# Optimization experiments

Measured on AMD Instinct MI355X. Metric: run time of the kernel, lower is better.

Reference implementation:

```python
import jax, jax.numpy as jnp
import numpy as np

H, T, D = 16, 2048, 1024
DH = D // H  # 64


def setup_inputs() -> dict:
    key = jax.random.key(0)
    ks = jax.random.split(key, 6)
    state = jax.random.normal(ks[0], (H, DH, DH), jnp.float32) * 0.02  # per-head recurrent state
    x = jax.random.normal(ks[1], (T, D), jnp.float32)
    done = jax.random.uniform(ks[2], (T,)) < (4.0 / T)  # sparse episode-reset flags (bool)
    w_qkv = jax.random.normal(ks[3], (D, 3 * D), jnp.float32) / np.sqrt(D)
    b_qkv = jnp.zeros((3 * D,), jnp.float32)
    w_out = jax.random.normal(ks[4], (D, D), jnp.float32) / np.sqrt(D)
    b_out = jnp.zeros((D,), jnp.float32)
    return {"state": state, "x": x, "done": done, "w_qkv": w_qkv,
            "b_qkv": b_qkv, "w_out": w_out, "b_out": b_out}


def _mha_forward(state, x, done, w_qkv, b_qkv, w_out, b_out):
    # qkv projection; einops 'T (QKV H Dh) -> QKV H T Dh'
    qkv = (x @ w_qkv + b_qkv).reshape(T, 3, H, DH).transpose(1, 2, 0, 3)
    q, k, v = qkv[0], qkv[1], qkv[2]  # each (H, T, Dh)

    cum = jnp.cumsum(done.astype(jnp.int32))  # inclusive cumsum, as in done.cumsum()
    before_first = cum == 0            # tokens before first reset (attend to carried state)
    after_last = cum == cum[-1]        # tokens after last reset (feed new state)
    done_any = cum[-1] > 0

    # make_attn_mask(done): causal AND no reset index i with s < i <= t.
    # The scanned mask equals: causal & (cum[t] == cum[s]) (same-segment).
    t_idx = jnp.arange(T)
    mask = (t_idx[:, None] >= t_idx[None, :]) & (cum[:, None] == cum[None, :])  # (T, T)

    attn = jnp.where(mask[None], jnp.einsum('htd,hsd->hts', q, k), 0.0)  # mask * (q @ k.T)
    q_bef = q * before_first[None, :, None]
    out = jnp.einsum('hts,hsd->htd', attn, v) + jnp.einsum('htd,hde->hte', q_bef, state)

    k_aft = k * after_last[None, :, None]
    v_aft = v * after_last[None, :, None]
    s_new = jnp.einsum('htd,hte->hde', k_aft, v_aft)  # k_aft.T @ v_aft per head
    new_state = jnp.where(done_any, s_new, state + s_new)

    # 'H T Dh -> T (H Dh)' then output projection
    x_out = out.transpose(1, 0, 2).reshape(T, D) @ w_out + b_out
    return new_state, x_out


def reference(state, x, done, w_qkv, b_qkv, w_out, b_out):
    return _mha_forward(state, x, done, w_qkv, b_qkv, w_out, b_out)
```

## Files before the change

### kernel.cpp

```cpp
#include <hip/hip_runtime.h>

#define TT 2048
#define DD 1024
#define HH 16
#define DH 64
#define QKV_N 3072
#define QKW 2048

typedef __attribute__((ext_vector_type(8))) short bf16x8;
typedef __attribute__((ext_vector_type(4))) short short4v;
typedef __attribute__((ext_vector_type(4))) float f32x4;

__device__ inline short f2bf(float f) {
    union { float f; unsigned u; } v; v.f = f;
    unsigned r = v.u + 0x7fff + ((v.u >> 16) & 1);
    return (short)(r >> 16);
}

__device__ inline f32x4 mfma16(bf16x8 a, bf16x8 b, f32x4 c) {
    return __builtin_amdgcn_mfma_f32_16x16x32_bf16(a, b, c, 0, 0, 0);
}

__device__ __forceinline__ void gload16(const void* g, void* l) {
    __builtin_amdgcn_global_load_lds(
        (const __attribute__((address_space(1))) unsigned int*)g,
        (__attribute__((address_space(3))) unsigned int*)l, 16, 0, 0);
}

__device__ void transpose_tile(const float* __restrict__ in, short* __restrict__ out,
                               int R, int C, int r0, int c0, float (*tile)[65]) {
    int tid = threadIdx.x;
#pragma unroll
    for (int p = 0; p < 4; ++p) {
        int ch = tid + p * 256;
        int r = ch >> 4, c4 = (ch & 15) * 4;
        float4 v = *(const float4*)&in[(size_t)(r0 + r) * C + c0 + c4];
        tile[r][c4] = v.x; tile[r][c4 + 1] = v.y; tile[r][c4 + 2] = v.z; tile[r][c4 + 3] = v.w;
    }
    __syncthreads();
#pragma unroll
    for (int p = 0; p < 2; ++p) {
        int ch = tid + p * 256;
        int c = ch >> 3, r8 = (ch & 7) * 8;
        short tmp[8];
#pragma unroll
        for (int i = 0; i < 8; ++i) tmp[i] = f2bf(tile[r8 + i][c]);
        *(float4*)&out[(size_t)(c0 + c) * R + r0 + r8] = *(float4*)tmp;
    }
}

__global__ __launch_bounds__(256) void prep_kernel(const float* __restrict__ x,
                                                   const float* __restrict__ w_qkv,
                                                   const float* __restrict__ w_out,
                                                   const float* __restrict__ state,
                                                   const int* __restrict__ done,
                                                   short* __restrict__ x_bf,
                                                   short* __restrict__ wqT,
                                                   short* __restrict__ woT,
                                                   short* __restrict__ stT,
                                                   float* __restrict__ stout,
                                                   int* __restrict__ seg,
                                                   int* __restrict__ totalp,
                                                   int* __restrict__ aux) {
    __shared__ float tile[64][65];
    __shared__ int scanbuf[2048 + 512 + 1];
    int b = blockIdx.x;
    int tid = threadIdx.x;
    if (b < 1024) {
        int i = (b * 256 + tid) * 8;
        float4 a = *(const float4*)&x[i];
        float4 c = *(const float4*)&x[i + 4];
        short tmp[8] = {f2bf(a.x), f2bf(a.y), f2bf(a.z), f2bf(a.w),
                        f2bf(c.x), f2bf(c.y), f2bf(c.z), f2bf(c.w)};
        *(float4*)&x_bf[i] = *(float4*)tmp;
    } else if (b < 1792) {
        int bb = b - 1024;
        transpose_tile(w_qkv, wqT, DD, QKV_N, (bb & 15) * 64, (bb >> 4) * 64, tile);
    } else if (b < 2048) {
        int bb = b - 1792;
        transpose_tile(w_out, woT, DD, DD, (bb & 15) * 64, (bb >> 4) * 64, tile);
    } else if (b < 2064) {
        int h = b - 2048;
        transpose_tile(state + (size_t)h * 4096, stT + (size_t)h * 4096, DH, DH, 0, 0, tile);
    } else if (b < 2128) {
        __shared__ int anyf;
        if (tid == 0) anyf = 0;
        __syncthreads();
        int acc = 0;
#pragma unroll
        for (int i = 0; i < 8; ++i) acc |= done[tid * 8 + i];
        if (acc) anyf = 1;
        __syncthreads();
        int f = ((b - 2064) * 256 + tid) * 4;
        float4 v = anyf ? make_float4(0.f, 0.f, 0.f, 0.f) : *(const float4*)&state[f];
        *(float4*)&stout[f] = v;
    } else {
        int* segl = scanbuf;
        int* part = scanbuf + 2048;
        int* excl = scanbuf + 2304;
        int base = tid * 8;
        int local[8];
        int run = 0;
#pragma unroll
        for (int i = 0; i < 8; ++i) { run += (done[base + i] != 0) ? 1 : 0; local[i] = run; }
        part[tid] = run;
        __syncthreads();
        if (tid < 64) {
            int p4[4];
#pragma unroll
            for (int i = 0; i < 4; ++i) p4[i] = part[tid * 4 + i];
            int s = p4[0] + p4[1] + p4[2] + p4[3];
            int v = s;
#pragma unroll
            for (int off = 1; off < 64; off <<= 1) {
                int u = __shfl_up(v, off);
                if (tid >= off) v += u;
            }
            int ex = v - s;
#pragma unroll
            for (int i = 0; i < 4; ++i) { excl[tid * 4 + i] = ex; ex += p4[i]; }
            if (tid == 63) { totalp[0] = v; scanbuf[2560] = v; }
        }
        __syncthreads();
        int off = excl[tid];
#pragma unroll
        for (int i = 0; i < 8; ++i) {
            int sv = off + local[i];
            seg[base + i] = sv;
            segl[base + i] = sv;
        }
        __syncthreads();
        if (tid < 33) {
            int target = (tid < 32) ? segl[tid * 64] : scanbuf[2560];
            int lo = 0, hi = 2047;
            while (lo < hi) { int mid = (lo + hi) >> 1; if (segl[mid] >= target) hi = mid; else lo = mid + 1; }
            aux[tid] = lo >> 6;
        }
    }
}

__global__ __launch_bounds__(256) void gemm_qkv(const short* __restrict__ A,
                                                const short* __restrict__ BT,
                                                const float* __restrict__ bias,
                                                short* __restrict__ qk,
                                                short* __restrict__ vt) {
    __shared__ __align__(16) short As[128 * 32];
    __shared__ __align__(16) short Bs[128 * 32];
    const int K = DD;
    int tid = threadIdx.x;
    int wave = tid >> 6, lane = tid & 63;
    int quad = lane >> 4, l15 = lane & 15;
    int m0 = blockIdx.x * 128, n0 = blockIdx.y * 128;
    int wr = (wave >> 1) * 64, wc = (wave & 1) * 64;

    int srow = wave * 16 + (lane >> 2);
    int scol = (lane & 3) * 8;
    const short* Ag = A + (size_t)(m0 + srow) * K + scol;
    const short* Bg = BT + (size_t)(n0 + srow) * K + scol;
    short* As0 = &As[(wave * 16) * 32];
    short* As1 = &As[(64 + wave * 16) * 32];
    short* Bs0 = &Bs[(wave * 16) * 32];
    short* Bs1 = &Bs[(64 + wave * 16) * 32];

    f32x4 acc[4][4] = {};
    for (int k0 = 0; k0 < K; k0 += 32) {
        __syncthreads();
        gload16(Ag + k0, As0);
        gload16(Ag + (size_t)64 * K + k0, As1);
        gload16(Bg + k0, Bs0);
        gload16(Bg + (size_t)64 * K + k0, Bs1);
        __syncthreads();
        bf16x8 af[4], bfr[4];
#pragma unroll
        for (int i = 0; i < 4; ++i) {
            af[i]  = *(const bf16x8*)&As[(wr + i * 16 + l15) * 32 + quad * 8];
            bfr[i] = *(const bf16x8*)&Bs[(wc + i * 16 + l15) * 32 + quad * 8];
        }
#pragma unroll
        for (int i = 0; i < 4; ++i)
#pragma unroll
            for (int j = 0; j < 4; ++j)
                acc[i][j] = mfma16(af[i], bfr[j], acc[i][j]);
    }

    if (n0 < 2048) {
#pragma unroll
        for (int i = 0; i < 4; ++i)
#pragma unroll
            for (int j = 0; j < 4; ++j)
#pragma unroll
                for (int r = 0; r < 4; ++r) {
                    int row = m0 + wr + i * 16 + quad * 4 + r;
                    int col = n0 + wc + j * 16 + l15;
                    qk[(size_t)row * QKW + col] = f2bf(acc[i][j][r] + bias[col]);
                }
    } else {
#pragma unroll
        for (int j = 0; j < 4; ++j) {
            int col = n0 + wc + j * 16 + l15;
            float bv = bias[col];
            int eg = col - 2048;
            int hh = eg >> 6, e = eg & 63;
#pragma unroll
            for (int i = 0; i < 4; ++i) {
                int tb = m0 + wr + i * 16 + quad * 4;
                short4v pk;
#pragma unroll
                for (int r = 0; r < 4; ++r) pk[r] = f2bf(acc[i][j][r] + bv);
                *(short4v*)&vt[(size_t)hh * (DH * TT) + (size_t)e * TT + tb] = pk;
            }
        }
    }
}

__global__ __launch_bounds__(256) void attn_mfma(const short* __restrict__ qk,
                                                 const short* __restrict__ vt,
                                                 const short* __restrict__ stT,
                                                 const int* __restrict__ seg,
                                                 const int* __restrict__ totalp,
                                                 const int* __restrict__ aux,
                                                 short* __restrict__ outb,
                                                 float* __restrict__ part,
                                                 float* __restrict__ nsout) {
    __shared__ __align__(16) short Kh[2][64 * 32];
    __shared__ __align__(16) short Vh[2][64 * 32];
    __shared__ __align__(16) short Qh[2][128 * 32];
    __shared__ __align__(16) short Ss[128 * 72];

    int h = blockIdx.x, tb = blockIdx.y, sc = blockIdx.z;
    int t0 = tb * 128;
    int tid = threadIdx.x, wave = tid >> 6, lane = tid & 63;
    int quad = lane >> 4, l15 = lane & 15;
    int myt = wave * 32;
    const short* vbase = vt + (size_t)h * (DH * TT);

    if (sc == 4) {
        int total = totalp[0];
        int myd = wave * 16;
#pragma unroll
        for (int cc = 0; cc < 2; ++cc) {
            int ct = tb * 2 + cc;
            if (ct < aux[32]) continue;
            int t0c = ct * 64;
            bool keep = (seg[t0c + lane] == total);
            const short* src = qk + (size_t)(t0c + lane) * QKW + 1024 + h * DH + myd;
            union { float4 f; short s[8]; } u0, u1;
            u0.f = keep ? *(const float4*)src : make_float4(0.f, 0.f, 0.f, 0.f);
            u1.f = keep ? *(const float4*)(src + 8) : make_float4(0.f, 0.f, 0.f, 0.f);
            short* dst = (lane < 32) ? &Kh[0][lane] : &Kh[1][lane - 32];
#pragma unroll
            for (int i = 0; i < 8; ++i) {
                dst[(myd + i) * 32] = u0.s[i];
                dst[(myd + 8 + i) * 32] = u1.s[i];
            }
            bf16x8 a0 = *(const bf16x8*)&Kh[0][(myd + l15) * 32 + quad * 8];
            bf16x8 a1 = *(const bf16x8*)&Kh[1][(myd + l15) * 32 + quad * 8];
            f32x4 acc2[4] = {};
#pragma unroll
            for (int j = 0; j < 4; ++j) {
                const short* vrow = vbase + (size_t)(j * 16 + l15) * TT + t0c + quad * 8;
                bf16x8 b0 = *(const bf16x8*)vrow;
                bf16x8 b1 = *(const bf16x8*)(vrow + 32);
                acc2[j] = mfma16(a0, b0, acc2[j]);
                acc2[j] = mfma16(a1, b1, acc2[j]);
            }
            float* oh = nsout + (size_t)h * 4096;
#pragma unroll
            for (int j = 0; j < 4; ++j)
#pragma unroll
                for (int r = 0; r < 4; ++r)
                    atomicAdd(&oh[(myd + quad * 4 + r) * DH + j * 16 + l15], acc2[j][r]);
        }
        return;
    }

    int st0 = aux[2 * tb];
    int sc_lo = st0 >> 3, sc_hi = (2 * tb + 1) >> 3;
    if (sc < sc_lo || sc > sc_hi) return;
    bool direct = (sc_lo == sc_hi);
    int st_lo = (st0 > sc * 8) ? st0 : sc * 8;
    int st_hi = (2 * tb + 1 < sc * 8 + 7) ? 2 * tb + 1 : sc * 8 + 7;

    {
        int srow = (lane >> 2);
        int chunk = (lane & 3);
#pragma unroll
        for (int h2 = 0; h2 < 2; ++h2)
#pragma unroll
            for (int q = 0; q < 2; ++q) {
                int row = myt + q * 16 + srow;
                gload16(qk + (size_t)(t0 + row) * QKW + h * DH + h2 * 32 + chunk * 8,
                        &Qh[h2][(myt + q * 16) * 32]);
            }
    }
    __syncthreads();

    bf16x8 af[2][2];
#pragma unroll
    for (int i = 0; i < 2; ++i)
#pragma unroll
        for (int h2 = 0; h2 < 2; ++h2)
            af[i][h2] = *(const bf16x8*)&Qh[h2][(myt + i * 16 + l15) * 32 + quad * 8];

    int tg[2][4], segt[2][4];
#pragma unroll
    for (int i = 0; i < 2; ++i)
#pragma unroll
        for (int r = 0; r < 4; ++r) {
            tg[i][r] = t0 + myt + i * 16 + quad * 4 + r;
            segt[i][r] = seg[tg[i][r]];
        }

    f32x4 acc[2][4] = {};
    if (sc == sc_lo && seg[t0] == 0) {
        const short* sb = stT + (size_t)h * 4096;
#pragma unroll
        for (int j = 0; j < 4; ++j)
#pragma unroll
            for (int h2 = 0; h2 < 2; ++h2) {
                bf16x8 b = *(const bf16x8*)(sb + (j * 16 + l15) * 64 + h2 * 32 + quad * 8);
#pragma unroll
                for (int i = 0; i < 2; ++i)
                    acc[i][j] = mfma16(af[i][h2], b, acc[i][j]);
            }
#pragma unroll
        for (int i = 0; i < 2; ++i)
#pragma unroll
            for (int r = 0; r < 4; ++r)
                if (segt[i][r] != 0)
#pragma unroll
                    for (int j = 0; j < 4; ++j) acc[i][j][r] = 0.f;
    }

    int srow = wave * 16 + (lane >> 2);
    int chunk = (lane & 3);
    const short* kg = qk + 1024 + h * DH;

    for (int st = st_lo; st <= st_hi; ++st) {
        int s0 = st * 64;
        __syncthreads();
        gload16(kg + (size_t)(s0 + srow) * QKW + chunk * 8,        &Kh[0][(wave * 16) * 32]);
        gload16(kg + (size_t)(s0 + srow) * QKW + 32 + chunk * 8,   &Kh[1][(wave * 16) * 32]);
        gload16(vbase + (size_t)srow * TT + s0 + chunk * 8,        &Vh[0][(wave * 16) * 32]);
        gload16(vbase + (size_t)srow * TT + s0 + 32 + chunk * 8,   &Vh[1][(wave * 16) * 32]);
        __syncthreads();

        int segs[4], sg[4];
#pragma unroll
        for (int j = 0; j < 4; ++j) { sg[j] = s0 + j * 16 + l15; segs[j] = seg[sg[j]]; }

        f32x4 sacc[2][4] = {};
#pragma unroll
        for (int j = 0; j < 4; ++j)
#pragma unroll
            for (int h2 = 0; h2 < 2; ++h2) {
                bf16x8 kb = *(const bf16x8*)&Kh[h2][(j * 16 + l15) * 32 + quad * 8];
#pragma unroll
                for (int i = 0; i < 2; ++i)
                    sacc[i][j] = mfma16(af[i][h2], kb, sacc[i][j]);
            }
#pragma unroll
        for (int i = 0; i < 2; ++i)
#pragma unroll
            for (int j = 0; j < 4; ++j)
#pragma unroll
                for (int r = 0; r < 4; ++r) {
                    bool ok = (segs[j] == segt[i][r]) && (sg[j] <= tg[i][r]);
                    Ss[(myt + i * 16 + quad * 4 + r) * 72 + j * 16 + l15] =
                        ok ? f2bf(sacc[i][j][r]) : (short)0;
                }
        bf16x8 sf[2][2];
#pragma unroll
        for (int i = 0; i < 2; ++i)
#pragma unroll
            for (int h2 = 0; h2 < 2; ++h2)
                sf[i][h2] = *(const bf16x8*)&Ss[(myt + i * 16 + l15) * 72 + h2 * 32 + quad * 8];
#pragma unroll
        for (int j = 0; j < 4; ++j)
#pragma unroll
            for (int h2 = 0; h2 < 2; ++h2) {
                bf16x8 vb = *(const bf16x8*)&Vh[h2][(j * 16 + l15) * 32 + quad * 8];
#pragma unroll
                for (int i = 0; i < 2; ++i)
                    acc[i][j] = mfma16(sf[i][h2], vb, acc[i][j]);
            }
    }

    if (direct) {
#pragma unroll
        for (int i = 0; i < 2; ++i)
#pragma unroll
            for (int j = 0; j < 4; ++j)
#pragma unroll
                for (int r = 0; r < 4; ++r)
                    outb[(size_t)tg[i][r] * DD + h * DH + j * 16 + l15] = f2bf(acc[i][j][r]);
    } else {
        float* pb = part + ((size_t)((h * 16 + tb) * 4 + sc)) * 8192;
#pragma unroll
        for (int i = 0; i < 2; ++i)
#pragma unroll
            for (int j = 0; j < 4; ++j)
#pragma unroll
                for (int r = 0; r < 4; ++r)
                    pb[(myt + i * 16 + quad * 4 + r) * 64 + j * 16 + l15] = acc[i][j][r];
    }
}

__global__ __launch_bounds__(256) void attn_reduce(const float* __restrict__ part,
                                                   const int* __restrict__ aux,
                                                   short* __restrict__ outb) {
    int h = blockIdx.x, tb = blockIdx.y;
    int sc_lo = aux[2 * tb] >> 3, sc_hi = (2 * tb + 1) >> 3;
    if (sc_lo == sc_hi) return;
    int t0 = tb * 128;
    int tid = threadIdx.x;
    const float* pb = part + ((size_t)(h * 16 + tb) * 4) * 8192;
#pragma unroll
    for (int p = 0; p < 8; ++p) {
        int idx = p * 256 + tid;
        int row = idx >> 4, c4 = (idx & 15) * 4;
        float4 acc = make_float4(0.f, 0.f, 0.f, 0.f);
        for (int sc = sc_lo; sc <= sc_hi; ++sc) {
            float4 v = *(const float4*)&pb[(size_t)sc * 8192 + row * 64 + c4];
            acc.x += v.x; acc.y += v.y; acc.z += v.z; acc.w += v.w;
        }
        short4v pk;
        pk[0] = f2bf(acc.x); pk[1] = f2bf(acc.y); pk[2] = f2bf(acc.z); pk[3] = f2bf(acc.w);
        *(short4v*)&outb[(size_t)(t0 + row) * DD + h * DH + c4] = pk;
    }
}

__global__ __launch_bounds__(256) void gemm_out(const short* __restrict__ A,
                                                const short* __restrict__ BT,
                                                const float* __restrict__ bias,
                                                float* __restrict__ Cout,
                                                int M, int N, int K) {
    __shared__ __align__(16) short As[128 * 32];
    __shared__ __align__(16) short Bs[128 * 32];
    int tid = threadIdx.x;
    int wave = tid >> 6, lane = tid & 63;
    int quad = lane >> 4, l15 = lane & 15;
    int m0 = blockIdx.x * 128, n0 = blockIdx.y * 128;
    int wr = (wave >> 1) * 64, wc = (wave & 1) * 64;

    int srow = wave * 16 + (lane >> 2);
    int scol = (lane & 3) * 8;
    const short* Ag = A + (size_t)(m0 + srow) * K + scol;
    const short* Bg = BT + (size_t)(n0 + srow) * K + scol;
    short* As0 = &As[(wave * 16) * 32];
    short* As1 = &As[(64 + wave * 16) * 32];
    short* Bs0 = &Bs[(wave * 16) * 32];
    short* Bs1 = &Bs[(64 + wave * 16) * 32];

    f32x4 acc[4][4] = {};
    for (int k0 = 0; k0 < K; k0 += 32) {
        __syncthreads();
        gload16(Ag + k0, As0);
        gload16(Ag + (size_t)64 * K + k0, As1);
        gload16(Bg + k0, Bs0);
        gload16(Bg + (size_t)64 * K + k0, Bs1);
        __syncthreads();
        bf16x8 af[4], bfr[4];
#pragma unroll
        for (int i = 0; i < 4; ++i) {
            af[i]  = *(const bf16x8*)&As[(wr + i * 16 + l15) * 32 + quad * 8];
            bfr[i] = *(const bf16x8*)&Bs[(wc + i * 16 + l15) * 32 + quad * 8];
        }
#pragma unroll
        for (int i = 0; i < 4; ++i)
#pragma unroll
            for (int j = 0; j < 4; ++j)
                acc[i][j] = mfma16(af[i], bfr[j], acc[i][j]);
    }
#pragma unroll
    for (int i = 0; i < 4; ++i)
#pragma unroll
        for (int j = 0; j < 4; ++j)
#pragma unroll
            for (int r = 0; r < 4; ++r) {
                int row = m0 + wr + i * 16 + quad * 4 + r;
                int col = n0 + wc + j * 16 + l15;
                Cout[(size_t)row * N + col] = acc[i][j][r] + bias[col];
            }
}

extern "C" void kernel_launch(void* const* d_in, const int* in_sizes, int n_in,
                              void* d_out, int out_size, void* d_ws, size_t ws_size,
                              hipStream_t stream) {
    const float* state = (const float*)d_in[0];
    const float* x     = (const float*)d_in[1];
    const int*   done  = (const int*)d_in[2];
    const float* w_qkv = (const float*)d_in[3];
    const float* b_qkv = (const float*)d_in[4];
    const float* w_out = (const float*)d_in[5];
    const float* b_out = (const float*)d_in[6];

    char* ws = (char*)d_ws;
    int*   seg    = (int*)ws;
    int*   totalp = (int*)(ws + 8192);
    int*   aux    = (int*)(ws + 8256);
    short* wqT    = (short*)(ws + 8448);
    short* woT    = (short*)(ws + 6299904);
    short* stT    = (short*)(ws + 8397056);
    short* qk     = (short*)(ws + 8528128);
    short* vt     = (short*)(ws + 16916736);
    short* xbf_outb = (short*)(ws + 21111040);
    float* part   = (float*)(ws + 25305344);

    float* new_state_out = (float*)d_out;
    float* x_out         = (float*)d_out + HH * DH * DH;

    prep_kernel<<<2129, 256, 0, stream>>>(x, w_qkv, w_out, state, done,
                                          xbf_outb, wqT, woT, stT,
                                          new_state_out, seg, totalp, aux);

    gemm_qkv<<<dim3(TT / 128, QKV_N / 128), 256, 0, stream>>>(
        xbf_outb, wqT, b_qkv, qk, vt);

    attn_mfma<<<dim3(HH, TT / 128, 5), 256, 0, stream>>>(
        qk, vt, stT, seg, totalp, aux, xbf_outb, part, new_state_out);

    attn_reduce<<<dim3(HH, TT / 128), 256, 0, stream>>>(part, aux, xbf_outb);

    gemm_out<<<dim3(TT / 128, DD / 128), 256, 0, stream>>>(
        xbf_outb, woT, b_out, x_out, TT, DD, DD);
}
```

Baseline: 161.9 us.

## Drop split-K attention partials and double-buffer K/V tiles in one pass

Removes the key-chunk split (grid z=5 with fp32 partials plus a separate reduce kernel). Each block now walks its whole key range in one pass and writes bf16 output directly. K/V tiles are double-buffered in shared memory so the next tile's loads overlap the current MFMA work. MFMA operands are swapped so the results come out transposed, which allows vectorized short4 stores and int4 segment loads. This saves one kernel launch and the partial-sum traffic, but long key ranges are no longer spread across blocks, which lowers parallelism for late query tiles.

Measured after the change: 163.5 us. Within noise of the previous version (+1.0%).

```diff
diff --git a/kernel.cpp b/kernel.cpp
--- a/kernel.cpp
+++ b/kernel.cpp
@@ -220,23 +220,24 @@
                                                  const int* __restrict__ totalp,
                                                  const int* __restrict__ aux,
                                                  short* __restrict__ outb,
-                                                 float* __restrict__ part,
                                                  float* __restrict__ nsout) {
-    __shared__ __align__(16) short Kh[2][64 * 32];
-    __shared__ __align__(16) short Vh[2][64 * 32];
     __shared__ __align__(16) short Qh[2][128 * 32];
+    __shared__ __align__(16) short Kh[2][2][64 * 32];
+    __shared__ __align__(16) short Vh[2][2][64 * 32];
     __shared__ __align__(16) short Ss[128 * 72];
 
-    int h = blockIdx.x, tb = blockIdx.y, sc = blockIdx.z;
+    int h = blockIdx.x, tb = blockIdx.y;
     int t0 = tb * 128;
     int tid = threadIdx.x, wave = tid >> 6, lane = tid & 63;
     int quad = lane >> 4, l15 = lane & 15;
     int myt = wave * 32;
     const short* vbase = vt + (size_t)h * (DH * TT);
 
-    if (sc == 4) {
+    if (blockIdx.z == 1) {
         int total = totalp[0];
         int myd = wave * 16;
+        short* KhS0 = Kh[0][0];
+        short* KhS1 = Kh[0][1];
 #pragma unroll
         for (int cc = 0; cc < 2; ++cc) {
             int ct = tb * 2 + cc;
@@ -247,14 +248,14 @@
             union { float4 f; short s[8]; } u0, u1;
             u0.f = keep ? *(const float4*)src : make_float4(0.f, 0.f, 0.f, 0.f);
             u1.f = keep ? *(const float4*)(src + 8) : make_float4(0.f, 0.f, 0.f, 0.f);
-            short* dst = (lane < 32) ? &Kh[0][lane] : &Kh[1][lane - 32];
+            short* dst = (lane < 32) ? &KhS0[lane] : &KhS1[lane - 32];
 #pragma unroll
             for (int i = 0; i < 8; ++i) {
                 dst[(myd + i) * 32] = u0.s[i];
                 dst[(myd + 8 + i) * 32] = u1.s[i];
             }
-            bf16x8 a0 = *(const bf16x8*)&Kh[0][(myd + l15) * 32 + quad * 8];
-            bf16x8 a1 = *(const bf16x8*)&Kh[1][(myd + l15) * 32 + quad * 8];
+            bf16x8 a0 = *(const bf16x8*)&KhS0[(myd + l15) * 32 + quad * 8];
+            bf16x8 a1 = *(const bf16x8*)&KhS1[(myd + l15) * 32 + quad * 8];
             f32x4 acc2[4] = {};
 #pragma unroll
             for (int j = 0; j < 4; ++j) {
@@ -275,100 +276,103 @@
     }
 
     int st0 = aux[2 * tb];
-    int sc_lo = st0 >> 3, sc_hi = (2 * tb + 1) >> 3;
-    if (sc < sc_lo || sc > sc_hi) return;
-    bool direct = (sc_lo == sc_hi);
-    int st_lo = (st0 > sc * 8) ? st0 : sc * 8;
-    int st_hi = (2 * tb + 1 < sc * 8 + 7) ? 2 * tb + 1 : sc * 8 + 7;
-
-    {
-        int srow = (lane >> 2);
-        int chunk = (lane & 3);
-#pragma unroll
-        for (int h2 = 0; h2 < 2; ++h2)
-#pragma unroll
-            for (int q = 0; q < 2; ++q) {
-                int row = myt + q * 16 + srow;
-                gload16(qk + (size_t)(t0 + row) * QKW + h * DH + h2 * 32 + chunk * 8,
-                        &Qh[h2][(myt + q * 16) * 32]);
-            }
-    }
-    __syncthreads();
-
-    bf16x8 af[2][2];
-#pragma unroll
-    for (int i = 0; i < 2; ++i)
-#pragma unroll
-        for (int h2 = 0; h2 < 2; ++h2)
-            af[i][h2] = *(const bf16x8*)&Qh[h2][(myt + i * 16 + l15) * 32 + quad * 8];
-
-    int tg[2][4], segt[2][4];
-#pragma unroll
-    for (int i = 0; i < 2; ++i)
-#pragma unroll
-        for (int r = 0; r < 4; ++r) {
-            tg[i][r] = t0 + myt + i * 16 + quad * 4 + r;
-            segt[i][r] = seg[tg[i][r]];
-        }
-
-    f32x4 acc[2][4] = {};
-    if (sc == sc_lo && seg[t0] == 0) {
-        const short* sb = stT + (size_t)h * 4096;
-#pragma unroll
-        for (int j = 0; j < 4; ++j)
-#pragma unroll
-            for (int h2 = 0; h2 < 2; ++h2) {
-                bf16x8 b = *(const bf16x8*)(sb + (j * 16 + l15) * 64 + h2 * 32 + quad * 8);
-#pragma unroll
-                for (int i = 0; i < 2; ++i)
-                    acc[i][j] = mfma16(af[i][h2], b, acc[i][j]);
-            }
-#pragma unroll
-        for (int i = 0; i < 2; ++i)
-#pragma unroll
-            for (int r = 0; r < 4; ++r)
-                if (segt[i][r] != 0)
-#pragma unroll
-                    for (int j = 0; j < 4; ++j) acc[i][j][r] = 0.f;
-    }
+    int st_hi = 2 * tb + 1;
 
     int srow = wave * 16 + (lane >> 2);
     int chunk = (lane & 3);
     const short* kg = qk + 1024 + h * DH;
 
-    for (int st = st_lo; st <= st_hi; ++st) {
+    {
+        int sr = (lane >> 2);
+#pragma unroll
+        for (int h2 = 0; h2 < 2; ++h2)
+#pragma unroll
+            for (int q = 0; q < 2; ++q)
+                gload16(qk + (size_t)(t0 + myt + q * 16 + sr) * QKW + h * DH + h2 * 32 + chunk * 8,
+                        &Qh[h2][(myt + q * 16) * 32]);
+        int s0 = st0 * 64;
+        gload16(kg + (size_t)(s0 + srow) * QKW + chunk * 8,      &Kh[0][0][(wave * 16) * 32]);
+        gload16(kg + (size_t)(s0 + srow) * QKW + 32 + chunk * 8, &Kh[0][1][(wave * 16) * 32]);
+        gload16(vbase + (size_t)srow * TT + s0 + chunk * 8,      &Vh[0][0][(wave * 16) * 32]);
+        gload16(vbase + (size_t)srow * TT + s0 + 32 + chunk * 8, &Vh[0][1][(wave * 16) * 32]);
+    }
+    __syncthreads();
+
+    bf16x8 af[2][2];
+#pragma unroll
+    for (int i = 0; i < 2; ++i)
+#pragma unroll
+        for (int h2 = 0; h2 < 2; ++h2)
+            af[i][h2] = *(const bf16x8*)&Qh[h2][(myt + i * 16 + l15) * 32 + quad * 8];
+
+    int seg_lane[2], t_val[2];
+#pragma unroll
+    for (int i = 0; i < 2; ++i) {
+        t_val[i] = t0 + myt + i * 16 + l15;
+        seg_lane[i] = seg[t_val[i]];
+    }
+
+    f32x4 acc2[4][2] = {};
+    if (seg[t0] == 0) {
+        const short* sb = stT + (size_t)h * 4096;
+#pragma unroll
+        for (int j = 0; j < 4; ++j)
+#pragma unroll
+            for (int h2 = 0; h2 < 2; ++h2) {
+                bf16x8 a = *(const bf16x8*)(sb + (j * 16 + l15) * 64 + h2 * 32 + quad * 8);
+#pragma unroll
+                for (int i = 0; i < 2; ++i)
+                    acc2[j][i] = mfma16(a, af[i][h2], acc2[j][i]);
+            }
+#pragma unroll
+        for (int i = 0; i < 2; ++i)
+            if (seg_lane[i] != 0)
+#pragma unroll
+                for (int j = 0; j < 4; ++j)
+#pragma unroll
+                    for (int r = 0; r < 4; ++r) acc2[j][i][r] = 0.f;
+    }
+
+    int p = 0;
+    for (int st = st0; st <= st_hi; ++st, p ^= 1) {
+        if (st != st0) __syncthreads();
+        if (st + 1 <= st_hi) {
+            int s1 = (st + 1) * 64;
+            gload16(kg + (size_t)(s1 + srow) * QKW + chunk * 8,      &Kh[p ^ 1][0][(wave * 16) * 32]);
+            gload16(kg + (size_t)(s1 + srow) * QKW + 32 + chunk * 8, &Kh[p ^ 1][1][(wave * 16) * 32]);
+            gload16(vbase + (size_t)srow * TT + s1 + chunk * 8,      &Vh[p ^ 1][0][(wave * 16) * 32]);
+            gload16(vbase + (size_t)srow * TT + s1 + 32 + chunk * 8, &Vh[p ^ 1][1][(wave * 16) * 32]);
+        }
         int s0 = st * 64;
-        __syncthreads();
-        gload16(kg + (size_t)(s0 + srow) * QKW + chunk * 8,        &Kh[0][(wave * 16) * 32]);
-        gload16(kg + (size_t)(s0 + srow) * QKW + 32 + chunk * 8,   &Kh[1][(wave * 16) * 32]);
-        gload16(vbase + (size_t)srow * TT + s0 + chunk * 8,        &Vh[0][(wave * 16) * 32]);
-        gload16(vbase + (size_t)srow * TT + s0 + 32 + chunk * 8,   &Vh[1][(wave * 16) * 32]);
-        __syncthreads();
-
-        int segs[4], sg[4];
-#pragma unroll
-        for (int j = 0; j < 4; ++j) { sg[j] = s0 + j * 16 + l15; segs[j] = seg[sg[j]]; }
 
         f32x4 sacc[2][4] = {};
 #pragma unroll
         for (int j = 0; j < 4; ++j)
 #pragma unroll
             for (int h2 = 0; h2 < 2; ++h2) {
-                bf16x8 kb = *(const bf16x8*)&Kh[h2][(j * 16 + l15) * 32 + quad * 8];
+                bf16x8 kb = *(const bf16x8*)&Kh[p][h2][(j * 16 + l15) * 32 + quad * 8];
 #pragma unroll
                 for (int i = 0; i < 2; ++i)
-                    sacc[i][j] = mfma16(af[i][h2], kb, sacc[i][j]);
-            }
+                    sacc[i][j] = mfma16(kb, af[i][h2], sacc[i][j]);
+            }
+        int4 seg4[4];
+#pragma unroll
+        for (int j = 0; j < 4; ++j)
+            seg4[j] = *(const int4*)&seg[s0 + j * 16 + quad * 4];
 #pragma unroll
         for (int i = 0; i < 2; ++i)
 #pragma unroll
-            for (int j = 0; j < 4; ++j)
+            for (int j = 0; j < 4; ++j) {
+                short4v pk;
 #pragma unroll
                 for (int r = 0; r < 4; ++r) {
-                    bool ok = (segs[j] == segt[i][r]) && (sg[j] <= tg[i][r]);
-                    Ss[(myt + i * 16 + quad * 4 + r) * 72 + j * 16 + l15] =
-                        ok ? f2bf(sacc[i][j][r]) : (short)0;
+                    int s_val = s0 + j * 16 + quad * 4 + r;
+                    int sv = (r == 0) ? seg4[j].x : (r == 1) ? seg4[j].y : (r == 2) ? seg4[j].z : seg4[j].w;
+                    bool ok = (sv == seg_lane[i]) && (s_val <= t_val[i]);
+                    pk[r] = ok ? f2bf(sacc[i][j][r]) : (short)0;
                 }
+                *(short4v*)&Ss[(myt + i * 16 + l15) * 72 + j * 16 + quad * 4] = pk;
+            }
         bf16x8 sf[2][2];
 #pragma unroll
         for (int i = 0; i < 2; ++i)
@@ -379,55 +383,22 @@
         for (int j = 0; j < 4; ++j)
 #pragma unroll
             for (int h2 = 0; h2 < 2; ++h2) {
-                bf16x8 vb = *(const bf16x8*)&Vh[h2][(j * 16 + l15) * 32 + quad * 8];
+                bf16x8 vb = *(const bf16x8*)&Vh[p][h2][(j * 16 + l15) * 32 + quad * 8];
 #pragma unroll
                 for (int i = 0; i < 2; ++i)
-                    acc[i][j] = mfma16(sf[i][h2], vb, acc[i][j]);
-            }
-    }
-
-    if (direct) {
-#pragma unroll
-        for (int i = 0; i < 2; ++i)
-#pragma unroll
-            for (int j = 0; j < 4; ++j)
-#pragma unroll
-                for (int r = 0; r < 4; ++r)
-                    outb[(size_t)tg[i][r] * DD + h * DH + j * 16 + l15] = f2bf(acc[i][j][r]);
-    } else {
-        float* pb = part + ((size_t)((h * 16 + tb) * 4 + sc)) * 8192;
-#pragma unroll
-        for (int i = 0; i < 2; ++i)
-#pragma unroll
-            for (int j = 0; j < 4; ++j)
-#pragma unroll
-                for (int r = 0; r < 4; ++r)
-                    pb[(myt + i * 16 + quad * 4 + r) * 64 + j * 16 + l15] = acc[i][j][r];
-    }
-}
-
-__global__ __launch_bounds__(256) void attn_reduce(const float* __restrict__ part,
-                                                   const int* __restrict__ aux,
-                                                   short* __restrict__ outb) {
-    int h = blockIdx.x, tb = blockIdx.y;
-    int sc_lo = aux[2 * tb] >> 3, sc_hi = (2 * tb + 1) >> 3;
-    if (sc_lo == sc_hi) return;
-    int t0 = tb * 128;
-    int tid = threadIdx.x;
-    const float* pb = part + ((size_t)(h * 16 + tb) * 4) * 8192;
-#pragma unroll
-    for (int p = 0; p < 8; ++p) {
-        int idx = p * 256 + tid;
-        int row = idx >> 4, c4 = (idx & 15) * 4;
-        float4 acc = make_float4(0.f, 0.f, 0.f, 0.f);
-        for (int sc = sc_lo; sc <= sc_hi; ++sc) {
-            float4 v = *(const float4*)&pb[(size_t)sc * 8192 + row * 64 + c4];
-            acc.x += v.x; acc.y += v.y; acc.z += v.z; acc.w += v.w;
-        }
-        short4v pk;
-        pk[0] = f2bf(acc.x); pk[1] = f2bf(acc.y); pk[2] = f2bf(acc.z); pk[3] = f2bf(acc.w);
-        *(short4v*)&outb[(size_t)(t0 + row) * DD + h * DH + c4] = pk;
-    }
+                    acc2[j][i] = mfma16(vb, sf[i][h2], acc2[j][i]);
+            }
+    }
+
+#pragma unroll
+    for (int i = 0; i < 2; ++i)
+#pragma unroll
+        for (int j = 0; j < 4; ++j) {
+            short4v pk;
+#pragma unroll
+            for (int r = 0; r < 4; ++r) pk[r] = f2bf(acc2[j][i][r]);
+            *(short4v*)&outb[(size_t)t_val[i] * DD + h * DH + j * 16 + quad * 4] = pk;
+        }
 }
 
 __global__ __launch_bounds__(256) void gemm_out(const short* __restrict__ A,
@@ -505,7 +476,6 @@
     short* qk     = (short*)(ws + 8528128);
     short* vt     = (short*)(ws + 16916736);
     short* xbf_outb = (short*)(ws + 21111040);
-    float* part   = (float*)(ws + 25305344);
 
     float* new_state_out = (float*)d_out;
     float* x_out         = (float*)d_out + HH * DH * DH;
@@ -517,10 +487,8 @@
     gemm_qkv<<<dim3(TT / 128, QKV_N / 128), 256, 0, stream>>>(
         xbf_outb, wqT, b_qkv, qk, vt);
 
-    attn_mfma<<<dim3(HH, TT / 128, 5), 256, 0, stream>>>(
-        qk, vt, stT, seg, totalp, aux, xbf_outb, part, new_state_out);
-
-    attn_reduce<<<dim3(HH, TT / 128), 256, 0, stream>>>(part, aux, xbf_outb);
+    attn_mfma<<<dim3(HH, TT / 128, 2), 256, 0, stream>>>(
+        qk, vt, stT, seg, totalp, aux, xbf_outb, new_state_out);
 
     gemm_out<<<dim3(TT / 128, DD / 128), 256, 0, stream>>>(
         xbf_outb, woT, b_out, x_out, TT, DD, DD);
```
